# Kernel optimization log

Hardware: AMD Instinct MI355X
Metric: run time of the kernel (lower is better)

## Reference

```python
import jax, jax.numpy as jnp
import numpy as np

N = 100000
E = 3_200_000
H = 64
R = 2
NEG = 0.01   # leaky_relu default slope
EPS = 1e-5   # BatchNorm eps


def leaky(x):
    return jnp.where(x > 0, x, NEG * x)


def bn(x, g, b, m, v):
    # BatchNorm1d in eval mode (running statistics)
    return (x - m) * jax.lax.rsqrt(v + EPS) * g + b


def setup_inputs() -> dict:
    key = jax.random.key(0)
    ks = jax.random.split(key, 16)
    d = {}
    d["des"] = jax.random.normal(ks[0], (N, 768), jnp.float32)
    d["num"] = jax.random.normal(ks[1], (N, 5), jnp.float32)
    d["cat"] = jax.random.normal(ks[2], (N, 6), jnp.float32)
    d["edge_index"] = jax.random.randint(ks[3], (2, E), 0, N)
    d["edge_type"] = jax.random.randint(ks[4], (E,), 0, R)

    def lin(k, o, i):
        return (jax.random.normal(k, (o, i), jnp.float32) / np.float32(np.sqrt(i)))

    # projection heads: Linear + BatchNorm1d params
    d["des_W"] = lin(ks[5], H, 768); d["des_b"] = jnp.zeros((H,), jnp.float32)
    d["num_W"] = lin(ks[6], H, 5);   d["num_b"] = jnp.zeros((H,), jnp.float32)
    d["cat_W"] = lin(ks[7], H, 6);   d["cat_b"] = jnp.zeros((H,), jnp.float32)
    for name, kk in (("des", ks[8]), ("num", ks[9]), ("cat", ks[10])):
        d[name + "_g"] = jnp.ones((H,), jnp.float32)
        d[name + "_beta"] = jnp.zeros((H,), jnp.float32)
        d[name + "_m"] = 0.1 * jax.random.normal(kk, (H,), jnp.float32)
        d[name + "_v"] = jnp.ones((H,), jnp.float32)
    # RGCN relation weights [R, in, out] (used as F.linear(x, W[r]) -> x @ W[r].T)
    d["rgcn_W"] = jax.random.normal(ks[11], (R, H, H), jnp.float32) / np.float32(np.sqrt(H))
    # classifier
    d["cls_W1"] = lin(ks[12], H // 2, H); d["cls_b1"] = jnp.zeros((H // 2,), jnp.float32)
    d["cls_W2"] = lin(ks[13], 2, H // 2); d["cls_b2"] = jnp.zeros((2,), jnp.float32)
    return d


def reference(des, num, cat, edge_index, edge_type,
              des_W, des_b, des_g, des_beta, des_m, des_v,
              num_W, num_b, num_g, num_beta, num_m, num_v,
              cat_W, cat_b, cat_g, cat_beta, cat_m, cat_v,
              rgcn_W, cls_W1, cls_b1, cls_W2, cls_b2):
    # feature fusion: three Linear+BN+LeakyReLU branches summed
    x = leaky(bn(des @ des_W.T + des_b, des_g, des_beta, des_m, des_v))
    x = x + leaky(bn(num @ num_W.T + num_b, num_g, num_beta, num_m, num_v))
    x = x + leaky(bn(cat @ cat_W.T + cat_b, cat_g, cat_beta, cat_m, cat_v))

    # SimpleRGCNConv: per-relation linear transform + masked scatter-mean over edges
    src, dst = edge_index[0], edge_index[1]  # PyG: row=source, col=target
    n = x.shape[0]
    acc = jnp.zeros((n, H), x.dtype)
    for r in range(R):
        x_r = x @ rgcn_W[r].T                       # F.linear(x, weight[r])
        mask = (edge_type == r).astype(x.dtype)     # [E]
        msg = x_r[src] * mask[:, None]              # gather + mask
        s = jax.ops.segment_sum(msg, dst, num_segments=n)
        cnt = jax.ops.segment_sum(mask, dst, num_segments=n)
        acc = acc + s / jnp.maximum(cnt, 1.0)[:, None]  # mean; 0 for isolated nodes
    x = leaky(acc / R)  # mean over relations

    # dropout in eval mode is identity; classifier
    h = leaky(x @ cls_W1.T + cls_b1)
    return h @ cls_W2.T + cls_b2
```

## Files before the change

### kernel.cpp

```cpp
#include <hip/hip_runtime.h>

typedef unsigned int u32;
typedef unsigned short u16;

#define NEG 0.01f
#define BN_EPS 1e-5f

typedef __attribute__((ext_vector_type(8))) short bf16x8;
typedef __attribute__((ext_vector_type(4))) float f32x4;

__device__ __forceinline__ float bl(u32 u){ union { u32 i; float f; } c; c.i = u << 16; return c.f; }
__device__ __forceinline__ float bh(u32 u){ union { u32 i; float f; } c; c.i = u & 0xFFFF0000u; return c.f; }
__device__ __forceinline__ float b2f(u16 u){ union { u32 i; float f; } c; c.i = ((u32)u) << 16; return c.f; }
__device__ __forceinline__ u16 f2b(float f){
  union { float f; u32 i; } c; c.f = f;
  u32 t = c.i + 0x7FFFu + ((c.i >> 16) & 1u);
  return (u16)(t >> 16);
}
__device__ __forceinline__ float leaky(float v){ return v > 0.f ? v : NEG * v; }

__global__ void k_prep(const float* __restrict__ desWf, const float* __restrict__ rgcnW,
                       const float* __restrict__ W1, u16* __restrict__ tab)
{
  int i = blockIdx.x * 256 + threadIdx.x;
  if (i < 49152) {
    tab[i] = f2b(desWf[i]);
  } else if (i < 57344) {
    int j = i - 49152;
    int h = j >> 7, k = j & 127;
    tab[i] = f2b(rgcnW[(k >= 64 ? 4096 : 0) + h * 64 + (k & 63)]);
  } else if (i < 59392) {
    tab[i] = f2b(W1[i - 57344]);
  }
}

__global__ __launch_bounds__(256) void k_fuse(
    const float* __restrict__ des, const float* __restrict__ nump, const float* __restrict__ catp,
    const u16* __restrict__ desW16, const float* __restrict__ desB,
    const float* __restrict__ numW, const float* __restrict__ numB,
    const float* __restrict__ catW, const float* __restrict__ catB,
    const float* __restrict__ dg, const float* __restrict__ dbe, const float* __restrict__ dm, const float* __restrict__ dv,
    const float* __restrict__ ng, const float* __restrict__ nbe, const float* __restrict__ nm, const float* __restrict__ nv,
    const float* __restrict__ cg, const float* __restrict__ cbe, const float* __restrict__ cm, const float* __restrict__ cv,
    u16* __restrict__ x16, int n)
{
  __shared__ float ync[64][66];

  const int tid  = threadIdx.x;
  const int lane = tid & 63;
  const int w    = tid >> 6;
  const int quad = lane >> 4;
  const int l15  = lane & 15;
  const int rowbase = blockIdx.x * 64 + 16 * w;

  {
    float nw[5], cw[6];
    #pragma unroll
    for (int j = 0; j < 5; ++j) nw[j] = numW[lane * 5 + j];
    #pragma unroll
    for (int j = 0; j < 6; ++j) cw[j] = catW[lane * 6 + j];
    float An = ng[lane] * rsqrtf(nv[lane] + BN_EPS);
    float Bn = (numB[lane] - nm[lane]) * An + nbe[lane];
    float Ac = cg[lane] * rsqrtf(cv[lane] + BN_EPS);
    float Bc = (catB[lane] - cm[lane]) * Ac + cbe[lane];
    for (int m = 0; m < 16; ++m) {
      int node = rowbase + m; if (node > n - 1) node = n - 1;
      float yn = 0.f, yc = 0.f;
      #pragma unroll
      for (int j = 0; j < 5; ++j) yn = fmaf(nump[node * 5 + j], nw[j], yn);
      #pragma unroll
      for (int j = 0; j < 6; ++j) yc = fmaf(catp[node * 6 + j], cw[j], yc);
      ync[16 * w + m][lane] = leaky(yn * An + Bn) + leaky(yc * Ac + Bc);
    }
  }

  float Ad4[4], Bd4[4];
  #pragma unroll
  for (int t = 0; t < 4; ++t) {
    int nn = 16 * t + l15;
    float A = dg[nn] * rsqrtf(dv[nn] + BN_EPS);
    Ad4[t] = A;
    Bd4[t] = (desB[nn] - dm[nn]) * A + dbe[nn];
  }
  __syncthreads();

  int rowA = rowbase + l15; if (rowA > n - 1) rowA = n - 1;
  const float* aP  = des + (size_t)rowA * 768 + quad * 8;
  const u16* b0P = desW16 + (size_t)(l15)      * 768 + quad * 8;
  const u16* b1P = desW16 + (size_t)(16 + l15) * 768 + quad * 8;
  const u16* b2P = desW16 + (size_t)(32 + l15) * 768 + quad * 8;
  const u16* b3P = desW16 + (size_t)(48 + l15) * 768 + quad * 8;

  f32x4 acc[4];
  #pragma unroll
  for (int t = 0; t < 4; ++t) acc[t] = (f32x4){0.f, 0.f, 0.f, 0.f};

  #pragma unroll 2
  for (int k = 0; k < 768; k += 32) {
    float4 x0 = *(const float4*)(aP + k);
    float4 x1 = *(const float4*)(aP + k + 4);
    bf16x8 a;
    a[0] = (short)f2b(x0.x); a[1] = (short)f2b(x0.y);
    a[2] = (short)f2b(x0.z); a[3] = (short)f2b(x0.w);
    a[4] = (short)f2b(x1.x); a[5] = (short)f2b(x1.y);
    a[6] = (short)f2b(x1.z); a[7] = (short)f2b(x1.w);
    acc[0] = __builtin_amdgcn_mfma_f32_16x16x32_bf16(a, *(const bf16x8*)(b0P + k), acc[0], 0, 0, 0);
    acc[1] = __builtin_amdgcn_mfma_f32_16x16x32_bf16(a, *(const bf16x8*)(b1P + k), acc[1], 0, 0, 0);
    acc[2] = __builtin_amdgcn_mfma_f32_16x16x32_bf16(a, *(const bf16x8*)(b2P + k), acc[2], 0, 0, 0);
    acc[3] = __builtin_amdgcn_mfma_f32_16x16x32_bf16(a, *(const bf16x8*)(b3P + k), acc[3], 0, 0, 0);
  }

  #pragma unroll
  for (int t = 0; t < 4; ++t) {
    #pragma unroll
    for (int r = 0; r < 4; ++r) {
      int m = quad * 4 + r;
      int node = rowbase + m;
      if (node < n) {
        int nn = 16 * t + l15;
        float v = leaky(acc[t][r] * Ad4[t] + Bd4[t]) + ync[16 * w + m][nn];
        x16[(size_t)node * 64 + nn] = f2b(v);
      }
    }
  }
}

__global__ void k_hist(const int* __restrict__ ei, const int* __restrict__ et,
                       int E, int* __restrict__ deg2)
{
  int e = blockIdx.x * 256 + threadIdx.x;
  if (e < E) atomicAdd(&deg2[ei[E + e] * 2 + et[e]], 1);
}

__global__ __launch_bounds__(1024) void k_scan(const int* __restrict__ deg2, int* __restrict__ offs2, int M)
{
  __shared__ int wsum[16];
  __shared__ int carry;
  const int tid = threadIdx.x, lane = tid & 63, w = tid >> 6;
  if (tid == 0) carry = 0;
  __syncthreads();
  for (int base = 0; base < M; base += 4096) {
    int idx = base + tid * 4;
    int4 v = {0, 0, 0, 0};
    if (idx < M) v = *(const int4*)(deg2 + idx);
    int s4 = v.x + v.y + v.z + v.w;
    int s = s4;
    #pragma unroll
    for (int o = 1; o < 64; o <<= 1) { int t = __shfl_up(s, o); if (lane >= o) s += t; }
    if (lane == 63) wsum[w] = s;
    __syncthreads();
    if (w == 0 && lane < 16) {
      int t = wsum[lane];
      #pragma unroll
      for (int o = 1; o < 16; o <<= 1) { int u = __shfl_up(t, o); if (lane >= o) t += u; }
      wsum[lane] = t;
    }
    __syncthreads();
    int wbase = (w == 0) ? 0 : wsum[w - 1];
    int ebase = carry + wbase + (s - s4);
    if (idx < M) {
      int4 o4;
      o4.x = ebase;
      o4.y = ebase + v.x;
      o4.z = ebase + v.x + v.y;
      o4.w = ebase + v.x + v.y + v.z;
      *(int4*)(offs2 + idx) = o4;
    }
    __syncthreads();
    if (tid == 0) carry += wsum[15];
    __syncthreads();
  }
  if (tid == 0) offs2[M] = carry;
}

__global__ void k_place(const int* __restrict__ ei, const int* __restrict__ et, int E,
                        const int* __restrict__ offs2, int* __restrict__ cur2, int* __restrict__ packed)
{
  int e = blockIdx.x * 256 + threadIdx.x;
  if (e < E) {
    int bin = ei[E + e] * 2 + et[e];
    int pos = offs2[bin] + atomicAdd(&cur2[bin], 1);
    packed[pos] = ei[e];
  }
}

__global__ __launch_bounds__(256) void k_agg(
    const u16* __restrict__ x16, const int* __restrict__ offs2, const int* __restrict__ packed,
    u32* __restrict__ agg, int n)
{
  const int tid = threadIdx.x, lane = tid & 63, w = tid >> 6;
  const int c = lane & 31, half = lane >> 5;

  for (int nd = blockIdx.x * 4 + w; nd < n; nd += gridDim.x * 4) {
    int o0 = offs2[nd * 2], o1 = offs2[nd * 2 + 1], o2 = offs2[nd * 2 + 2];
    float aE[2], aO[2];

    #pragma unroll
    for (int rel = 0; rel < 2; ++rel) {
      int beg = rel ? o1 : o0;
      int end = rel ? o2 : o1;
      float accE = 0.f, accO = 0.f;
      for (int j0 = beg; j0 < end; j0 += 64) {
        int idx = j0 + lane;
        int p = (idx < end) ? packed[idx] : 0;
        p = (p < 0) ? 0 : ((p > n - 1) ? (n - 1) : p);
        int cn = end - j0; if (cn > 64) cn = 64;
        int t = 0;
        for (; t + 8 <= cn; t += 8) {
          int s0 = __shfl(p, t     + half);
          int s1 = __shfl(p, t + 2 + half);
          int s2 = __shfl(p, t + 4 + half);
          int s3 = __shfl(p, t + 6 + half);
          u32 v0 = *(const u32*)(x16 + (size_t)s0 * 64 + 2 * c);
          u32 v1 = *(const u32*)(x16 + (size_t)s1 * 64 + 2 * c);
          u32 v2 = *(const u32*)(x16 + (size_t)s2 * 64 + 2 * c);
          u32 v3 = *(const u32*)(x16 + (size_t)s3 * 64 + 2 * c);
          accE += (bl(v0) + bl(v1)) + (bl(v2) + bl(v3));
          accO += (bh(v0) + bh(v1)) + (bh(v2) + bh(v3));
        }
        for (; t + 2 <= cn; t += 2) {
          int s0 = __shfl(p, t + half);
          u32 v0 = *(const u32*)(x16 + (size_t)s0 * 64 + 2 * c);
          accE += bl(v0); accO += bh(v0);
        }
        if (t < cn) {
          int s0 = __shfl(p, t);
          if (half == 0) {
            u32 v0 = *(const u32*)(x16 + (size_t)s0 * 64 + 2 * c);
            accE += bl(v0); accO += bh(v0);
          }
        }
      }
      accE += __shfl_xor(accE, 32);
      accO += __shfl_xor(accO, 32);
      int cnt = end - beg;
      float sc = 1.f / (float)(cnt > 1 ? cnt : 1);
      aE[rel] = accE * sc;
      aO[rel] = accO * sc;
    }

    float sE = half ? aE[1] : aE[0];
    float sO = half ? aO[1] : aO[0];
    agg[(size_t)nd * 64 + lane] = (u32)f2b(sE) | ((u32)f2b(sO) << 16);
  }
}

__global__ __launch_bounds__(256) void k_mlp(
    const u32* __restrict__ agg, const u16* __restrict__ Wmlp, const u16* __restrict__ W1p,
    const float* __restrict__ b1, const float* __restrict__ W2, const float* __restrict__ b2,
    float2* __restrict__ out, int n)
{
  __shared__ __align__(16) u16 h1[4][16][72];
  __shared__ float h2[4][16][34];

  const int tid = threadIdx.x, lane = tid & 63, w = tid >> 6;
  const int quad = lane >> 4, l15 = lane & 15;
  const int rowbase = blockIdx.x * 64 + 16 * w;

  int rowA = rowbase + l15; if (rowA > n - 1) rowA = n - 1;
  const u16* aRow = (const u16*)(agg + (size_t)rowA * 64);

  f32x4 acc[4];
  #pragma unroll
  for (int t = 0; t < 4; ++t) acc[t] = (f32x4){0.f, 0.f, 0.f, 0.f};
  #pragma unroll
  for (int ks = 0; ks < 4; ++ks) {
    bf16x8 a = *(const bf16x8*)(aRow + ks * 32 + quad * 8);
    #pragma unroll
    for (int t = 0; t < 4; ++t) {
      bf16x8 b = *(const bf16x8*)(Wmlp + (size_t)(16 * t + l15) * 128 + ks * 32 + quad * 8);
      acc[t] = __builtin_amdgcn_mfma_f32_16x16x32_bf16(a, b, acc[t], 0, 0, 0);
    }
  }
  #pragma unroll
  for (int t = 0; t < 4; ++t)
    #pragma unroll
    for (int r = 0; r < 4; ++r) {
      int m = quad * 4 + r;
      h1[w][m][16 * t + l15] = f2b(leaky(0.5f * acc[t][r]));
    }
  __syncthreads();

  f32x4 acc2[2];
  acc2[0] = (f32x4){0.f, 0.f, 0.f, 0.f};
  acc2[1] = (f32x4){0.f, 0.f, 0.f, 0.f};
  #pragma unroll
  for (int ks = 0; ks < 2; ++ks) {
    bf16x8 a = *(const bf16x8*)(&h1[w][l15][ks * 32 + quad * 8]);
    #pragma unroll
    for (int t = 0; t < 2; ++t) {
      bf16x8 b = *(const bf16x8*)(W1p + (size_t)(16 * t + l15) * 64 + ks * 32 + quad * 8);
      acc2[t] = __builtin_amdgcn_mfma_f32_16x16x32_bf16(a, b, acc2[t], 0, 0, 0);
    }
  }
  #pragma unroll
  for (int t = 0; t < 2; ++t)
    #pragma unroll
    for (int r = 0; r < 4; ++r) {
      int m = quad * 4 + r;
      int j = 16 * t + l15;
      h2[w][m][j] = leaky(acc2[t][r] + b1[j]);
    }
  __syncthreads();

  float t0 = 0.f, t1 = 0.f;
  #pragma unroll
  for (int jj = 0; jj < 8; ++jj) {
    int j = quad * 8 + jj;
    float hv = h2[w][l15][j];
    t0 = fmaf(hv, W2[j], t0);
    t1 = fmaf(hv, W2[32 + j], t1);
  }
  t0 += __shfl_xor(t0, 16); t0 += __shfl_xor(t0, 32);
  t1 += __shfl_xor(t1, 16); t1 += __shfl_xor(t1, 32);
  int node = rowbase + l15;
  if (quad == 0 && node < n) {
    float2 q; q.x = t0 + b2[0]; q.y = t1 + b2[1];
    out[node] = q;
  }
}

extern "C" void kernel_launch(void* const* d_in, const int* in_sizes, int n_in,
                              void* d_out, int out_size, void* d_ws, size_t ws_size,
                              hipStream_t stream)
{
  const float* des  = (const float*)d_in[0];
  const float* nump = (const float*)d_in[1];
  const float* catp = (const float*)d_in[2];
  const int* ei   = (const int*)d_in[3];
  const int* et   = (const int*)d_in[4];
  const float* desW = (const float*)d_in[5];
  const float* desB = (const float*)d_in[6];
  const float* numW = (const float*)d_in[7];
  const float* numB = (const float*)d_in[8];
  const float* catW = (const float*)d_in[9];
  const float* catB = (const float*)d_in[10];
  const float* dg  = (const float*)d_in[11];
  const float* dbe = (const float*)d_in[12];
  const float* dm  = (const float*)d_in[13];
  const float* dv  = (const float*)d_in[14];
  const float* ng  = (const float*)d_in[15];
  const float* nbe = (const float*)d_in[16];
  const float* nm  = (const float*)d_in[17];
  const float* nv  = (const float*)d_in[18];
  const float* cg  = (const float*)d_in[19];
  const float* cbe = (const float*)d_in[20];
  const float* cm  = (const float*)d_in[21];
  const float* cv  = (const float*)d_in[22];
  const float* rgcnW = (const float*)d_in[23];
  const float* W1 = (const float*)d_in[24];
  const float* b1 = (const float*)d_in[25];
  const float* W2 = (const float*)d_in[26];
  const float* b2 = (const float*)d_in[27];

  const int N = in_sizes[1] / 5;
  const int E = in_sizes[4];
  const int M = 2 * N;

  char* ws = (char*)d_ws;
  u16* tab    = (u16*)ws;                  size_t off = (size_t)59392 * 2;
  off = (off + 255) & ~(size_t)255;
  u16* x16    = (u16*)(ws + off);          off += (size_t)N * 64 * 2;
  u32* agg    = (u32*)(ws + off);          off += (size_t)N * 64 * 4;
  int* deg2   = (int*)(ws + off);          off += (size_t)M * 4;
  int* cur2   = (int*)(ws + off);          off += (size_t)M * 4;
  int* offs2  = (int*)(ws + off);          off += (size_t)(M + 1) * 4;
  off = (off + 255) & ~(size_t)255;
  int* packed = (int*)(ws + off);

  u16* desW16 = tab;
  u16* Wmlp   = tab + 49152;
  u16* W1p    = tab + 57344;

  hipMemsetAsync(deg2, 0, (size_t)M * 8, stream);

  k_prep<<<(59392 + 255) / 256, 256, 0, stream>>>(desW, rgcnW, W1, tab);
  k_fuse<<<(N + 63) / 64, 256, 0, stream>>>(des, nump, catp, desW16, desB, numW, numB, catW, catB,
                                            dg, dbe, dm, dv, ng, nbe, nm, nv, cg, cbe, cm, cv,
                                            x16, N);
  k_hist<<<(E + 255) / 256, 256, 0, stream>>>(ei, et, E, deg2);
  k_scan<<<1, 1024, 0, stream>>>(deg2, offs2, M);
  k_place<<<(E + 255) / 256, 256, 0, stream>>>(ei, et, E, offs2, cur2, packed);
  k_agg<<<2048, 256, 0, stream>>>(x16, offs2, packed, agg, N);
  k_mlp<<<(N + 63) / 64, 256, 0, stream>>>(agg, Wmlp, W1p, b1, W2, b2, (float2*)d_out, N);
}
```

Before: 942.3 us.

## Merge histogram with weight prep and overlap scan with fusion kernel

Folds the weight bf16 conversion into the edge-histogram kernel and runs the degree prefix scan in block 0 of the feature-fusion kernel, so the serial single-block scan overlaps with the dense fusion work and two launches are removed. The scan block now uses 256 threads instead of 1024, so it takes more iterations. The aggregation loop also gains a 16-way unrolled gather to keep more loads in flight. The catch is that the scan block can become the critical path if the fusion blocks finish before it.

```diff
diff --git a/kernel.cpp b/kernel.cpp
--- a/kernel.cpp
+++ b/kernel.cpp
@@ -11,7 +11,6 @@
 
 __device__ __forceinline__ float bl(u32 u){ union { u32 i; float f; } c; c.i = u << 16; return c.f; }
 __device__ __forceinline__ float bh(u32 u){ union { u32 i; float f; } c; c.i = u & 0xFFFF0000u; return c.f; }
-__device__ __forceinline__ float b2f(u16 u){ union { u32 i; float f; } c; c.i = ((u32)u) << 16; return c.f; }
 __device__ __forceinline__ u16 f2b(float f){
   union { float f; u32 i; } c; c.f = f;
   u32 t = c.i + 0x7FFFu + ((c.i >> 16) & 1u);
@@ -19,22 +18,31 @@
 }
 __device__ __forceinline__ float leaky(float v){ return v > 0.f ? v : NEG * v; }
 
-__global__ void k_prep(const float* __restrict__ desWf, const float* __restrict__ rgcnW,
-                       const float* __restrict__ W1, u16* __restrict__ tab)
-{
-  int i = blockIdx.x * 256 + threadIdx.x;
-  if (i < 49152) {
-    tab[i] = f2b(desWf[i]);
-  } else if (i < 57344) {
-    int j = i - 49152;
-    int h = j >> 7, k = j & 127;
-    tab[i] = f2b(rgcnW[(k >= 64 ? 4096 : 0) + h * 64 + (k & 63)]);
-  } else if (i < 59392) {
-    tab[i] = f2b(W1[i - 57344]);
-  }
-}
-
-__global__ __launch_bounds__(256) void k_fuse(
+__global__ __launch_bounds__(256) void k_hist_prep(
+    const int* __restrict__ ei, const int* __restrict__ et, int E, int HB,
+    int* __restrict__ deg2,
+    const float* __restrict__ desWf, const float* __restrict__ rgcnW,
+    const float* __restrict__ W1, u16* __restrict__ tab)
+{
+  int bid = blockIdx.x;
+  if (bid < HB) {
+    int e = bid * 256 + threadIdx.x;
+    if (e < E) atomicAdd(&deg2[ei[E + e] * 2 + et[e]], 1);
+  } else {
+    int i = (bid - HB) * 256 + threadIdx.x;
+    if (i < 49152) {
+      tab[i] = f2b(desWf[i]);
+    } else if (i < 57344) {
+      int j = i - 49152;
+      int h = j >> 7, k = j & 127;
+      tab[i] = f2b(rgcnW[(k >= 64 ? 4096 : 0) + h * 64 + (k & 63)]);
+    } else if (i < 59392) {
+      tab[i] = f2b(W1[i - 57344]);
+    }
+  }
+}
+
+__global__ __launch_bounds__(256) void k_fuse_scan(
     const float* __restrict__ des, const float* __restrict__ nump, const float* __restrict__ catp,
     const u16* __restrict__ desW16, const float* __restrict__ desB,
     const float* __restrict__ numW, const float* __restrict__ numB,
@@ -42,16 +50,58 @@
     const float* __restrict__ dg, const float* __restrict__ dbe, const float* __restrict__ dm, const float* __restrict__ dv,
     const float* __restrict__ ng, const float* __restrict__ nbe, const float* __restrict__ nm, const float* __restrict__ nv,
     const float* __restrict__ cg, const float* __restrict__ cbe, const float* __restrict__ cm, const float* __restrict__ cv,
-    u16* __restrict__ x16, int n)
-{
-  __shared__ float ync[64][66];
-
+    u16* __restrict__ x16, int n,
+    const int* __restrict__ deg2, int* __restrict__ offs2, int M)
+{
   const int tid  = threadIdx.x;
   const int lane = tid & 63;
   const int w    = tid >> 6;
+
+  if (blockIdx.x == 0) {
+    __shared__ int wsum[4];
+    __shared__ int carry;
+    if (tid == 0) carry = 0;
+    __syncthreads();
+    for (int base = 0; base < M; base += 1024) {
+      int idx = base + tid * 4;
+      int4 v = {0, 0, 0, 0};
+      if (idx < M) v = *(const int4*)(deg2 + idx);
+      int s4 = v.x + v.y + v.z + v.w;
+      int s = s4;
+      #pragma unroll
+      for (int o = 1; o < 64; o <<= 1) { int t = __shfl_up(s, o); if (lane >= o) s += t; }
+      if (lane == 63) wsum[w] = s;
+      __syncthreads();
+      if (tid == 0) {
+        int a = wsum[0];
+        a += wsum[1]; wsum[1] = a;
+        a += wsum[2]; wsum[2] = a;
+        a += wsum[3]; wsum[3] = a;
+      }
+      __syncthreads();
+      int wbase = (w == 0) ? 0 : wsum[w - 1];
+      int ebase = carry + wbase + (s - s4);
+      if (idx < M) {
+        int4 o4;
+        o4.x = ebase;
+        o4.y = ebase + v.x;
+        o4.z = ebase + v.x + v.y;
+        o4.w = ebase + v.x + v.y + v.z;
+        *(int4*)(offs2 + idx) = o4;
+      }
+      __syncthreads();
+      if (tid == 0) carry += wsum[3];
+      __syncthreads();
+    }
+    if (tid == 0) offs2[M] = carry;
+    return;
+  }
+
+  __shared__ float ync[64][66];
+
   const int quad = lane >> 4;
   const int l15  = lane & 15;
-  const int rowbase = blockIdx.x * 64 + 16 * w;
+  const int rowbase = (blockIdx.x - 1) * 64 + 16 * w;
 
   {
     float nw[5], cw[6];
@@ -125,54 +175,6 @@
   }
 }
 
-__global__ void k_hist(const int* __restrict__ ei, const int* __restrict__ et,
-                       int E, int* __restrict__ deg2)
-{
-  int e = blockIdx.x * 256 + threadIdx.x;
-  if (e < E) atomicAdd(&deg2[ei[E + e] * 2 + et[e]], 1);
-}
-
-__global__ __launch_bounds__(1024) void k_scan(const int* __restrict__ deg2, int* __restrict__ offs2, int M)
-{
-  __shared__ int wsum[16];
-  __shared__ int carry;
-  const int tid = threadIdx.x, lane = tid & 63, w = tid >> 6;
-  if (tid == 0) carry = 0;
-  __syncthreads();
-  for (int base = 0; base < M; base += 4096) {
-    int idx = base + tid * 4;
-    int4 v = {0, 0, 0, 0};
-    if (idx < M) v = *(const int4*)(deg2 + idx);
-    int s4 = v.x + v.y + v.z + v.w;
-    int s = s4;
-    #pragma unroll
-    for (int o = 1; o < 64; o <<= 1) { int t = __shfl_up(s, o); if (lane >= o) s += t; }
-    if (lane == 63) wsum[w] = s;
-    __syncthreads();
-    if (w == 0 && lane < 16) {
-      int t = wsum[lane];
-      #pragma unroll
-      for (int o = 1; o < 16; o <<= 1) { int u = __shfl_up(t, o); if (lane >= o) t += u; }
-      wsum[lane] = t;
-    }
-    __syncthreads();
-    int wbase = (w == 0) ? 0 : wsum[w - 1];
-    int ebase = carry + wbase + (s - s4);
-    if (idx < M) {
-      int4 o4;
-      o4.x = ebase;
-      o4.y = ebase + v.x;
-      o4.z = ebase + v.x + v.y;
-      o4.w = ebase + v.x + v.y + v.z;
-      *(int4*)(offs2 + idx) = o4;
-    }
-    __syncthreads();
-    if (tid == 0) carry += wsum[15];
-    __syncthreads();
-  }
-  if (tid == 0) offs2[M] = carry;
-}
-
 __global__ void k_place(const int* __restrict__ ei, const int* __restrict__ et, int E,
                         const int* __restrict__ offs2, int* __restrict__ cur2, int* __restrict__ packed)
 {
@@ -206,6 +208,26 @@
         p = (p < 0) ? 0 : ((p > n - 1) ? (n - 1) : p);
         int cn = end - j0; if (cn > 64) cn = 64;
         int t = 0;
+        for (; t + 16 <= cn; t += 16) {
+          int s0 = __shfl(p, t      + half);
+          int s1 = __shfl(p, t + 2  + half);
+          int s2 = __shfl(p, t + 4  + half);
+          int s3 = __shfl(p, t + 6  + half);
+          int s4 = __shfl(p, t + 8  + half);
+          int s5 = __shfl(p, t + 10 + half);
+          int s6 = __shfl(p, t + 12 + half);
+          int s7 = __shfl(p, t + 14 + half);
+          u32 v0 = *(const u32*)(x16 + (size_t)s0 * 64 + 2 * c);
+          u32 v1 = *(const u32*)(x16 + (size_t)s1 * 64 + 2 * c);
+          u32 v2 = *(const u32*)(x16 + (size_t)s2 * 64 + 2 * c);
+          u32 v3 = *(const u32*)(x16 + (size_t)s3 * 64 + 2 * c);
+          u32 v4 = *(const u32*)(x16 + (size_t)s4 * 64 + 2 * c);
+          u32 v5 = *(const u32*)(x16 + (size_t)s5 * 64 + 2 * c);
+          u32 v6 = *(const u32*)(x16 + (size_t)s6 * 64 + 2 * c);
+          u32 v7 = *(const u32*)(x16 + (size_t)s7 * 64 + 2 * c);
+          accE += ((bl(v0) + bl(v1)) + (bl(v2) + bl(v3))) + ((bl(v4) + bl(v5)) + (bl(v6) + bl(v7)));
+          accO += ((bh(v0) + bh(v1)) + (bh(v2) + bh(v3))) + ((bh(v4) + bh(v5)) + (bh(v6) + bh(v7)));
+        }
         for (; t + 8 <= cn; t += 8) {
           int s0 = __shfl(p, t     + half);
           int s1 = __shfl(p, t + 2 + half);
@@ -374,12 +396,15 @@
 
   hipMemsetAsync(deg2, 0, (size_t)M * 8, stream);
 
-  k_prep<<<(59392 + 255) / 256, 256, 0, stream>>>(desW, rgcnW, W1, tab);
-  k_fuse<<<(N + 63) / 64, 256, 0, stream>>>(des, nump, catp, desW16, desB, numW, numB, catW, catB,
-                                            dg, dbe, dm, dv, ng, nbe, nm, nv, cg, cbe, cm, cv,
-                                            x16, N);
-  k_hist<<<(E + 255) / 256, 256, 0, stream>>>(ei, et, E, deg2);
-  k_scan<<<1, 1024, 0, stream>>>(deg2, offs2, M);
+  const int HB = (E + 255) / 256;
+  const int PB = (59392 + 255) / 256;
+  k_hist_prep<<<HB + PB, 256, 0, stream>>>(ei, et, E, HB, deg2, desW, rgcnW, W1, tab);
+
+  const int FB = (N + 63) / 64;
+  k_fuse_scan<<<FB + 1, 256, 0, stream>>>(des, nump, catp, desW16, desB, numW, numB, catW, catB,
+                                          dg, dbe, dm, dv, ng, nbe, nm, nv, cg, cbe, cm, cv,
+                                          x16, N, deg2, offs2, M);
+
   k_place<<<(E + 255) / 256, 256, 0, stream>>>(ei, et, E, offs2, cur2, packed);
   k_agg<<<2048, 256, 0, stream>>>(x16, offs2, packed, agg, N);
   k_mlp<<<(N + 63) / 64, 256, 0, stream>>>(agg, Wmlp, W1p, b1, W2, b2, (float2*)d_out, N);
```

After: 951.4 us. Within noise of the previous version (+1.0%).
